# Kernel tuning notes

Measured on AMD Instinct MI355X. Metric: run time of the kernel, lower is better.

Reference implementation:

```python
import jax, jax.numpy as jnp
import numpy as np

B, S, D, H = 4, 2048, 512, 8
HD = D // H


def rotate_half(t):
    half = t.shape[-1] // 2
    return jnp.concatenate([-t[..., half:], t[..., :half]], axis=-1)


def setup_inputs() -> dict:
    key = jax.random.key(0)
    ks = jax.random.split(key, 8)
    x = jax.random.normal(ks[0], (B, S, D), dtype=jnp.float32)
    # realistic rotary tables built from angles
    inv_freq = 1.0 / (10000.0 ** (jnp.arange(0, D // 2, dtype=jnp.float32) / (D // 2)))
    ang = jnp.arange(S, dtype=jnp.float32)[:, None] * inv_freq[None, :]  # [S, D/2]
    ang = jnp.concatenate([ang, ang], axis=-1)  # [S, D]
    cos_emb = jnp.cos(ang)[None]  # [1, S, D]
    sin_emb = jnp.sin(ang)[None]
    mask = jax.random.randint(ks[1], (B, S, S), 0, 2).astype(jnp.bool_)
    scale = 1.0 / np.sqrt(D)
    wq = jax.random.normal(ks[2], (D, D), dtype=jnp.float32) * scale
    wk = jax.random.normal(ks[3], (D, D), dtype=jnp.float32) * scale
    wv = jax.random.normal(ks[4], (D, D), dtype=jnp.float32) * scale
    wo = jax.random.normal(ks[5], (D, D), dtype=jnp.float32) * scale
    return {"x": x, "cos_emb": cos_emb, "sin_emb": sin_emb, "mask": mask,
            "wq": wq, "wk": wk, "wv": wv, "wo": wo}


def reference(x, cos_emb, sin_emb, mask, wq, wk, wv, wo):
    bsz, seqlen, dim = x.shape
    # projections (weights stored as [in, out])
    xq = x @ wq
    xk = x @ wk
    xv = x @ wv
    # RoPE applied over full dim before head split (as in original)
    xq = xq * cos_emb + rotate_half(xq) * sin_emb
    xk = xk * cos_emb + rotate_half(xk) * sin_emb
    # split heads: [B, H, S, HD]
    xq = xq.reshape(bsz, seqlen, H, HD).transpose(0, 2, 1, 3)
    xk = xk.reshape(bsz, seqlen, H, HD).transpose(0, 2, 1, 3)
    xv = xv.reshape(bsz, seqlen, H, HD).transpose(0, 2, 1, 3)
    scores = jnp.einsum('bhqd,bhkd->bhqk', xq, xk) / jnp.sqrt(jnp.float32(HD))
    scores = scores + (~mask)[:, None].astype(scores.dtype) * (-1e9)
    scores = jax.nn.softmax(scores.astype(jnp.float32), axis=-1).astype(xq.dtype)
    scores = scores * mask[:, None].astype(scores.dtype)
    out = jnp.einsum('bhqk,bhkd->bhqd', scores, xv)
    out = out.transpose(0, 2, 1, 3).reshape(bsz, seqlen, dim)
    return out @ wo
```

## Files before the change

### kernel.cpp

```cpp
#include <hip/hip_runtime.h>
#include <hip/hip_bf16.h>

typedef __bf16 bf16x8 __attribute__((ext_vector_type(8)));
typedef float f32x4 __attribute__((ext_vector_type(4)));
typedef short short8 __attribute__((ext_vector_type(8)));

#define MFMA16(a, b, c) __builtin_amdgcn_mfma_f32_16x16x32_bf16((a), (b), (c), 0, 0, 0)

static constexpr int S = 2048;
static constexpr int D = 512;
static constexpr int HD = 64;
static constexpr int KBLK = 64;
#define QSCALE 0.18033688011112042f

typedef __attribute__((address_space(1))) const unsigned int gu32;
typedef __attribute__((address_space(3))) unsigned int lu32;

__device__ __forceinline__ void gll16(const void* g, void* l) {
  __builtin_amdgcn_global_load_lds((gu32*)g, (lu32*)l, 16, 0, 0);
}

__device__ __forceinline__ unsigned short f2b(float f) {
  return __builtin_bit_cast(unsigned short, __float2bfloat16(f));
}
__device__ __forceinline__ float b2f(unsigned short u) {
  return __builtin_bit_cast(float, (unsigned)u << 16);
}

__global__ void prep_kernel(const float* __restrict__ x, unsigned short* __restrict__ xb,
                            const int* __restrict__ m, unsigned long long* __restrict__ bits,
                            const float* __restrict__ wq, const float* __restrict__ wk,
                            const float* __restrict__ wv, const float* __restrict__ wo,
                            unsigned short* __restrict__ wqkvT, unsigned short* __restrict__ woT) {
  __shared__ float t[64][65];
  const int blk = blockIdx.x;
  const int tid = threadIdx.x;
  if (blk < 4096) {
    int idx = blk * 256 + tid;
    float4 v = ((const float4*)x)[idx];
    ushort4 o;
    o.x = f2b(v.x); o.y = f2b(v.y); o.z = f2b(v.z); o.w = f2b(v.w);
    ((ushort4*)xb)[idx] = o;
  } else if (blk < 6144) {
    const int stride = 2048 * 256;
    const int lane0 = (tid & 63) == 0;
    for (int gid = (blk - 4096) * 256 + tid; gid < 4 * 2048 * 2048; gid += stride) {
      unsigned long long w = __ballot(m[gid] != 0);
      if (lane0) bits[gid >> 6] = w;
    }
  } else {
    const int tt = blk - 6144;
    const int z = tt >> 6, r = tt & 63;
    const float* w = (z == 0) ? wq : (z == 1) ? wk : (z == 2) ? wv : wo;
    unsigned short* dst = (z < 3) ? wqkvT + (size_t)z * 512 * 512 : woT;
    const int i0 = (r & 7) * 64, o0 = (r >> 3) * 64;
    for (int it = 0; it < 16; ++it) {
      int idx = it * 256 + tid;
      int ii = idx >> 6, oo = idx & 63;
      t[oo][ii] = w[(size_t)(i0 + ii) * 512 + o0 + oo];
    }
    __syncthreads();
    for (int it = 0; it < 16; ++it) {
      int idx = it * 256 + tid;
      int oo = idx >> 6, ii = idx & 63;
      dst[(size_t)(o0 + oo) * 512 + i0 + ii] = f2b(t[oo][ii]);
    }
  }
}

__global__ __launch_bounds__(256)
void gemm2(const unsigned short* __restrict__ A, const unsigned short* __restrict__ Bt,
           int M, int N, int K, float* __restrict__ Cf,
           unsigned short* __restrict__ qd, unsigned short* __restrict__ kd,
           unsigned short* __restrict__ vtd, int mode) {
  __shared__ alignas(16) unsigned char smem[36864];
  unsigned short (*lds)[2][4096] = (unsigned short (*)[2][4096])smem;
  const int tid = threadIdx.x;
  const int lane = tid & 63, l15 = lane & 15, lg = lane >> 4;
  const int wave = tid >> 6;
  const int m0 = blockIdx.x * 128, n0 = blockIdx.y * 128;
  const int wm = (wave >> 1) * 64, wn = (wave & 1) * 64;
  const int wbase = wave * 512;
  const int grow = tid >> 2, gcol = (tid & 3) * 8;
  f32x4 acc[4][4] = {};
  const int nt = K / 32;

#define GSTAGE(sb, kk)                                                              \
  do {                                                                              \
    gll16(&A[(size_t)(m0 + grow) * K + (kk) + gcol], &lds[sb][0][wbase]);           \
    gll16(&A[(size_t)(m0 + 64 + grow) * K + (kk) + gcol], &lds[sb][0][2048 + wbase]);\
    gll16(&Bt[(size_t)(n0 + grow) * K + (kk) + gcol], &lds[sb][1][wbase]);          \
    gll16(&Bt[(size_t)(n0 + 64 + grow) * K + (kk) + gcol], &lds[sb][1][2048 + wbase]);\
  } while (0)

  GSTAGE(0, 0);
  asm volatile("s_waitcnt vmcnt(0)" ::: "memory");
  __syncthreads();
  for (int t = 0; t < nt; ++t) {
    const int cur = t & 1;
    if (t + 1 < nt) GSTAGE(cur ^ 1, (t + 1) * 32);
    bf16x8 af[4], bfr[4];
#pragma unroll
    for (int i = 0; i < 4; ++i) {
      af[i]  = *(const bf16x8*)&lds[cur][0][(wm + i * 16 + l15) * 32 + lg * 8];
      bfr[i] = *(const bf16x8*)&lds[cur][1][(wn + i * 16 + l15) * 32 + lg * 8];
    }
    __builtin_amdgcn_s_setprio(1);
#pragma unroll
    for (int i = 0; i < 4; ++i)
#pragma unroll
      for (int j = 0; j < 4; ++j)
        acc[i][j] = MFMA16(af[i], bfr[j], acc[i][j]);
    __builtin_amdgcn_s_setprio(0);
    asm volatile("s_waitcnt vmcnt(0)" ::: "memory");
    __syncthreads();
  }
#undef GSTAGE

  if (mode == 0) {
#pragma unroll
    for (int i = 0; i < 4; ++i)
#pragma unroll
      for (int j = 0; j < 4; ++j)
#pragma unroll
        for (int r = 0; r < 4; ++r)
          Cf[(size_t)(m0 + wm + i * 16 + lg * 4 + r) * N + (n0 + wn + j * 16 + l15)] = acc[i][j][r];
  } else {
    const int sel = n0 >> 9;
    const int nb = (n0 & 511) + wn;
    if (sel < 2) {
      unsigned short* dst = (sel == 0) ? qd : kd;
#pragma unroll
      for (int i = 0; i < 4; ++i)
#pragma unroll
        for (int j = 0; j < 4; ++j)
#pragma unroll
          for (int r = 0; r < 4; ++r) {
            const int m = m0 + wm + i * 16 + lg * 4 + r;
            const int nn = nb + j * 16 + l15;
            dst[(((size_t)(m >> 11) * 8 + (nn >> 6)) * 2048 + (m & 2047)) * 64 + (nn & 63)] =
                f2b(acc[i][j][r]);
          }
    } else {
      unsigned short* tb = (unsigned short*)smem + wave * 4608;
#pragma unroll
      for (int i = 0; i < 4; ++i)
#pragma unroll
        for (int j = 0; j < 4; ++j) {
          ushort4 pk;
          pk.x = f2b(acc[i][j][0]); pk.y = f2b(acc[i][j][1]);
          pk.z = f2b(acc[i][j][2]); pk.w = f2b(acc[i][j][3]);
          *(ushort4*)&tb[(j * 16 + l15) * 72 + i * 16 + lg * 4] = pk;
        }
      const int b0 = m0 >> 11;
      const int s0 = (m0 & 2047) + wm;
      const int g = lane >> 3, c = lane & 7;
#pragma unroll
      for (int rr = 0; rr < 8; ++rr) {
        const int row = rr * 8 + g;
        const int nng = nb + row;
        uint4 v = *(const uint4*)&tb[row * 72 + c * 8];
        *(uint4*)&vtd[(((size_t)(b0 * 8) + (nng >> 6)) * 64 + (nng & 63)) * 2048 + s0 + c * 8] = v;
      }
    }
  }
}

__global__ void rope_pair_kernel(const unsigned short* __restrict__ qpre, const unsigned short* __restrict__ kpre,
                                 const float* __restrict__ cose, const float* __restrict__ sine,
                                 unsigned short* __restrict__ qb, unsigned short* __restrict__ kb) {
  const int idx = blockIdx.x * 256 + threadIdx.x;
  const int hd0 = (idx & 7) * 8;
  const int rr = idx >> 3;
  const int b = rr >> 13, h = (rr >> 11) & 3, s = rr & 2047;
  const size_t lo = ((size_t)(b * 8 + h) * 2048 + s) * 64 + hd0;
  const size_t hi = lo + (size_t)4 * 2048 * 64;
  const int d0 = h * 64 + hd0;
  short8 qlo = *(const short8*)&qpre[lo];
  short8 qhi = *(const short8*)&qpre[hi];
  short8 klo = *(const short8*)&kpre[lo];
  short8 khi = *(const short8*)&kpre[hi];
  float4 c0 = *(const float4*)&cose[(size_t)s * 512 + d0];
  float4 c1 = *(const float4*)&cose[(size_t)s * 512 + d0 + 4];
  float4 s0 = *(const float4*)&sine[(size_t)s * 512 + d0];
  float4 s1 = *(const float4*)&sine[(size_t)s * 512 + d0 + 4];
  float cc[8] = {c0.x, c0.y, c0.z, c0.w, c1.x, c1.y, c1.z, c1.w};
  float ss[8] = {s0.x, s0.y, s0.z, s0.w, s1.x, s1.y, s1.z, s1.w};
  short8 qolo, qohi, kolo, kohi;
#pragma unroll
  for (int j = 0; j < 8; ++j) {
    float ql = b2f((unsigned short)qlo[j]), qh = b2f((unsigned short)qhi[j]);
    float kl = b2f((unsigned short)klo[j]), kh = b2f((unsigned short)khi[j]);
    qolo[j] = (short)f2b((ql * cc[j] - qh * ss[j]) * QSCALE);
    qohi[j] = (short)f2b((qh * cc[j] + ql * ss[j]) * QSCALE);
    kolo[j] = (short)f2b(kl * cc[j] - kh * ss[j]);
    kohi[j] = (short)f2b(kh * cc[j] + kl * ss[j]);
  }
  *(short8*)&qb[lo] = qolo;
  *(short8*)&qb[hi] = qohi;
  *(short8*)&kb[lo] = kolo;
  *(short8*)&kb[hi] = kohi;
}

__global__ __launch_bounds__(512)
void flash_kernel(const unsigned short* __restrict__ qb, const unsigned short* __restrict__ kb,
                  const unsigned short* __restrict__ vtb, const unsigned long long* __restrict__ mbits,
                  unsigned short* __restrict__ op0, unsigned short* __restrict__ op1,
                  float* __restrict__ ls0, float* __restrict__ ls1) {
  __shared__ alignas(16) unsigned short kv[2][2][4096];
  __shared__ alignas(16) f32x4 btab[16];
  const int tid = threadIdx.x;
  const int wave = tid >> 6, lane = tid & 63;
  const int l15 = lane & 15, lg = lane >> 4;
  const int swz = (l15 & 7) << 4;
  const int wgid = blockIdx.x;
  const int slot = wgid >> 3;
  const int bh = (wgid & 7) * 4 + (slot & 3);
  const int rest = slot >> 2;
  const int kh = rest & 1;
  const int q0 = (rest >> 1) * 256 + wave * 16;
  const int b = bh >> 3, h = bh & 7;
  const int kbase = kh * 1024;
  const unsigned short* Q = qb + ((size_t)bh * S + q0) * HD;
  const unsigned short* Kp = kb + (size_t)bh * S * HD;
  const unsigned short* Vt = vtb + (size_t)bh * HD * S;
  const unsigned long long* MrowA = mbits + ((size_t)b * S + q0 + l15) * (S / 64) + kh * 16;
  const unsigned long long* MrowB = MrowA + (size_t)128 * (S / 64);
  unsigned short* opart = kh ? op1 : op0;
  float* lsum = kh ? ls1 : ls0;

  const int srow = tid >> 3;
  const int scol = ((tid & 7) ^ (srow & 7)) * 8;
  const int ksrow = ((srow & 15) >> 2) * 8 + ((srow >> 4) & 1) * 4 + (srow & 3) + (srow >> 5) * 32;
  const int wbase = wave * 512;

  if (tid < 16) {
    f32x4 e;
    e[0] = (tid & 1) ? 0.f : -300.f;
    e[1] = (tid & 2) ? 0.f : -300.f;
    e[2] = (tid & 4) ? 0.f : -300.f;
    e[3] = (tid & 8) ? 0.f : -300.f;
    btab[tid] = e;
  }

  bf16x8 qf0a = *(const bf16x8*)&Q[l15 * HD + lg * 8];
  bf16x8 qf1a = *(const bf16x8*)&Q[l15 * HD + 32 + lg * 8];
  bf16x8 qf0b = *(const bf16x8*)&Q[(128 + l15) * HD + lg * 8];
  bf16x8 qf1b = *(const bf16x8*)&Q[(128 + l15) * HD + 32 + lg * 8];
  f32x4 oa[4] = {}, ob[4] = {};
  float lpa = 0.f, lpb = 0.f;
  const int lgs8 = lg * 8;

  unsigned long long wAa = MrowA[0], wAb = MrowB[0];
  gll16(&Kp[(size_t)(kbase + ksrow) * HD + scol], &kv[0][0][wbase]);
  gll16(&Vt[(size_t)srow * S + kbase + scol], &kv[0][1][wbase]);
  asm volatile("s_waitcnt vmcnt(0) lgkmcnt(0)" ::: "memory");
  __syncthreads();

  for (int t = 0; t < 16; ++t) {
    const int cur = t & 1;
    unsigned long long wBa = 0, wBb = 0;
    if (t + 1 < 16) {
      const int kn = kbase + (t + 1) * KBLK;
      gll16(&Kp[(size_t)(kn + ksrow) * HD + scol], &kv[cur ^ 1][0][wbase]);
      gll16(&Vt[(size_t)srow * S + kn + scol], &kv[cur ^ 1][1][wbase]);
      wBa = MrowA[t + 1];
      wBb = MrowB[t + 1];
    }
    const char* kbp = (const char*)&kv[cur][0][0];
    const char* vbp = (const char*)&kv[cur][1][0];

    bf16x8 pf0a, pf1a, pf0b, pf1b;
#pragma unroll
    for (int n = 0; n < 4; ++n) {
      const int cb = (n * 16 + l15) * 128 + ((lg * 16) ^ swz);
      bf16x8 kf0 = *(const bf16x8*)(kbp + cb);
      bf16x8 kf1 = *(const bf16x8*)(kbp + (cb ^ 64));
      f32x4 scA = {}, scB = {};
      __builtin_amdgcn_s_setprio(1);
      scA = MFMA16(kf0, qf0a, scA);
      scA = MFMA16(kf1, qf1a, scA);
      scB = MFMA16(kf0, qf0b, scB);
      scB = MFMA16(kf1, qf1b, scB);
      __builtin_amdgcn_s_setprio(0);
      const int sh = (n == 0) ? 0 : (n == 1) ? 4 : (n == 2) ? 32 : 36;
      const f32x4 ba = btab[(unsigned)(wAa >> (lgs8 + sh)) & 15u];
      const f32x4 bb = btab[(unsigned)(wAb >> (lgs8 + sh)) & 15u];
      f32x4 pa, pb;
#pragma unroll
      for (int r = 0; r < 4; ++r) {
        pa[r] = __builtin_amdgcn_exp2f(scA[r] + ba[r]);
        pb[r] = __builtin_amdgcn_exp2f(scB[r] + bb[r]);
      }
      lpa += (pa[0] + pa[1]) + (pa[2] + pa[3]);
      lpb += (pb[0] + pb[1]) + (pb[2] + pb[3]);
      bf16x8& dsta = (n < 2) ? pf0a : pf1a;
      bf16x8& dstb = (n < 2) ? pf0b : pf1b;
      const int jo = (n & 1) * 4;
#pragma unroll
      for (int j = 0; j < 4; ++j) {
        dsta[jo + j] = (__bf16)pa[j];
        dstb[jo + j] = (__bf16)pb[j];
      }
    }

    __builtin_amdgcn_s_setprio(1);
#pragma unroll
    for (int n = 0; n < 4; ++n) {
      const int cb = (n * 16 + l15) * 128 + ((lg * 16) ^ swz);
      bf16x8 vf0 = *(const bf16x8*)(vbp + cb);
      bf16x8 vf1 = *(const bf16x8*)(vbp + (cb ^ 64));
      oa[n] = MFMA16(pf0a, vf0, oa[n]);
      oa[n] = MFMA16(pf1a, vf1, oa[n]);
      ob[n] = MFMA16(pf0b, vf0, ob[n]);
      ob[n] = MFMA16(pf1b, vf1, ob[n]);
    }
    __builtin_amdgcn_s_setprio(0);

    asm volatile("s_waitcnt vmcnt(0)" ::: "memory");
    __syncthreads();
    wAa = wBa;
    wAb = wBb;
  }

  lpa += __shfl_xor(lpa, 16);
  lpa += __shfl_xor(lpa, 32);
  lpb += __shfl_xor(lpb, 16);
  lpb += __shfl_xor(lpb, 32);
  if (lg == 0) {
    lsum[(size_t)bh * S + q0 + l15] = lpa;
    lsum[(size_t)bh * S + q0 + 128 + l15] = lpb;
  }
#pragma unroll
  for (int r = 0; r < 4; ++r)
#pragma unroll
    for (int n = 0; n < 4; ++n) {
      opart[((size_t)(b * S + q0 + lg * 4 + r)) * D + h * HD + n * 16 + l15] = f2b(oa[n][r]);
      opart[((size_t)(b * S + q0 + 128 + lg * 4 + r)) * D + h * HD + n * 16 + l15] = f2b(ob[n][r]);
    }
}

__global__ __launch_bounds__(256)
void gemm_fused(const unsigned short* __restrict__ op0, const unsigned short* __restrict__ op1,
                const float* __restrict__ ls0, const float* __restrict__ ls1,
                const unsigned short* __restrict__ Bt, float* __restrict__ C) {
  __shared__ alignas(16) unsigned short ldsA[2][2048];
  __shared__ alignas(16) unsigned short ldsB[2][4096];
  __shared__ float invt[512];
  const int tid = threadIdx.x;
  const int lane = tid & 63, l15 = lane & 15, lg = lane >> 4;
  const int wave = tid >> 6;
  const int m0 = blockIdx.x * 64, n0 = blockIdx.y * 128;
  const int wm = (wave >> 1) * 32, wn = (wave & 1) * 64;
  const int wbase = wave * 512;
  const int grow = tid >> 2, gcol = (tid & 3) * 8;
  const size_t abase = (size_t)(m0 + (tid >> 2)) * 512 + (tid & 3) * 8;
  f32x4 acc[2][4] = {};

  for (int e = tid; e < 512; e += 256) {
    const int row = e >> 3, hh = e & 7;
    const int m = m0 + row;
    const size_t li = ((size_t)((m >> 11) * 8 + hh)) * 2048 + (m & 2047);
    const float l = ls0[li] + ls1[li];
    invt[e] = (l > 0.f) ? 1.f / l : 0.f;
  }

#define BSTAGE(sb, kk)                                                               \
  do {                                                                               \
    gll16(&Bt[(size_t)(n0 + grow) * 512 + (kk) + gcol], &ldsB[sb][wbase]);           \
    gll16(&Bt[(size_t)(n0 + 64 + grow) * 512 + (kk) + gcol], &ldsB[sb][2048 + wbase]);\
  } while (0)

  short8 a8, p8;
#define ALOAD(kk)                                          \
  do {                                                     \
    a8 = *(const short8*)&op0[abase + (kk)];               \
    p8 = *(const short8*)&op1[abase + (kk)];               \
  } while (0)

#define AWRITE(sb, kk)                                                                   \
  do {                                                                                   \
    const float inv = invt[((tid >> 2) << 3) | ((kk) >> 6)];                             \
    short8 pk;                                                                           \
    pk[0] = (short)f2b((b2f((unsigned short)a8[0]) + b2f((unsigned short)p8[0])) * inv); \
    pk[1] = (short)f2b((b2f((unsigned short)a8[1]) + b2f((unsigned short)p8[1])) * inv); \
    pk[2] = (short)f2b((b2f((unsigned short)a8[2]) + b2f((unsigned short)p8[2])) * inv); \
    pk[3] = (short)f2b((b2f((unsigned short)a8[3]) + b2f((unsigned short)p8[3])) * inv); \
    pk[4] = (short)f2b((b2f((unsigned short)a8[4]) + b2f((unsigned short)p8[4])) * inv); \
    pk[5] = (short)f2b((b2f((unsigned short)a8[5]) + b2f((unsigned short)p8[5])) * inv); \
    pk[6] = (short)f2b((b2f((unsigned short)a8[6]) + b2f((unsigned short)p8[6])) * inv); \
    pk[7] = (short)f2b((b2f((unsigned short)a8[7]) + b2f((unsigned short)p8[7])) * inv); \
    *(short8*)&ldsA[sb][(tid >> 2) * 32 + (tid & 3) * 8] = pk;                           \
  } while (0)

  ALOAD(0);
  BSTAGE(0, 0);
  __syncthreads();
  AWRITE(0, 0);
  __syncthreads();

  for (int t = 0; t < 16; ++t) {
    const int cur = t & 1;
    const bool have = (t + 1 < 16);
    if (have) { ALOAD((t + 1) * 32); BSTAGE(cur ^ 1, (t + 1) * 32); }
    bf16x8 af[2], bfr[4];
#pragma unroll
    for (int i = 0; i < 2; ++i)
      af[i] = *(const bf16x8*)&ldsA[cur][(wm + i * 16 + l15) * 32 + lg * 8];
#pragma unroll
    for (int j = 0; j < 4; ++j)
      bfr[j] = *(const bf16x8*)&ldsB[cur][(wn + j * 16 + l15) * 32 + lg * 8];
    __builtin_amdgcn_s_setprio(1);
#pragma unroll
    for (int i = 0; i < 2; ++i)
#pragma unroll
      for (int j = 0; j < 4; ++j)
        acc[i][j] = MFMA16(af[i], bfr[j], acc[i][j]);
    __builtin_amdgcn_s_setprio(0);
    asm volatile("s_waitcnt vmcnt(0)" ::: "memory");
    __syncthreads();
    if (have) AWRITE(cur ^ 1, (t + 1) * 32);
    __syncthreads();
  }
#undef BSTAGE
#undef ALOAD
#undef AWRITE

#pragma unroll
  for (int i = 0; i < 2; ++i)
#pragma unroll
    for (int j = 0; j < 4; ++j)
#pragma unroll
      for (int r = 0; r < 4; ++r)
        C[(size_t)(m0 + wm + i * 16 + lg * 4 + r) * 512 + (n0 + wn + j * 16 + l15)] = acc[i][j][r];
}

extern "C" void kernel_launch(void* const* d_in, const int* in_sizes, int n_in,
                              void* d_out, int out_size, void* d_ws, size_t ws_size,
                              hipStream_t stream) {
  const float* x = (const float*)d_in[0];
  const float* cose = (const float*)d_in[1];
  const float* sine = (const float*)d_in[2];
  const int* mask = (const int*)d_in[3];
  const float* wq = (const float*)d_in[4];
  const float* wk = (const float*)d_in[5];
  const float* wv = (const float*)d_in[6];
  const float* wo = (const float*)d_in[7];
  float* out = (float*)d_out;
  char* ws = (char*)d_ws;

  unsigned short* xb    = (unsigned short*)(ws);
  unsigned short* wqkvT = (unsigned short*)(ws + 8388608);
  unsigned short* woT   = (unsigned short*)(ws + 9961472);
  unsigned short* qpre  = (unsigned short*)(ws + 10485760);
  unsigned short* kpre  = (unsigned short*)(ws + 18874368);
  unsigned short* qbh   = (unsigned short*)(ws + 35651584);
  unsigned short* kbh   = (unsigned short*)(ws + 44040192);
  unsigned short* vtb   = (unsigned short*)(ws + 52428800);
  unsigned long long* mbits = (unsigned long long*)(ws + 60817408);
  unsigned short* op0 = (unsigned short*)(ws + 10485760);
  unsigned short* op1 = (unsigned short*)(ws + 62914560);
  float* ls0 = (float*)(ws + 79691776);
  float* ls1 = (float*)(ws + 79953920);

  prep_kernel<<<6400, 256, 0, stream>>>(x, xb, mask, mbits, wq, wk, wv, wo, wqkvT, woT);
  gemm2<<<dim3(64, 12), 256, 0, stream>>>(xb, wqkvT, 8192, 1536, 512, nullptr, qpre, kpre, vtb, 1);
  rope_pair_kernel<<<1024, 256, 0, stream>>>(qpre, kpre, cose, sine, qbh, kbh);
  flash_kernel<<<512, 512, 0, stream>>>(qbh, kbh, vtb, mbits, op0, op1, ls0, ls1);
  gemm_fused<<<dim3(128, 4), 256, 0, stream>>>(op0, op1, ls0, ls1, woT, out);
}
```

Baseline: 111.6 us.

## Fuse RoPE into QKV GEMM epilogue via permuted weight columns

Permutes the Q/K weight output columns during prep so that each GEMM wave tile holds both rotate-half partners of a dimension. RoPE and the Q scale are then applied in the GEMM epilogue, and the separate rope kernel is removed. This drops one launch and the bf16 round-trip of pre-RoPE Q/K through global memory. In exchange the epilogue does scalar, less coalesced cos/sin loads and 2-byte scattered stores.

```diff
diff --git a/kernel.cpp b/kernel.cpp
--- a/kernel.cpp
+++ b/kernel.cpp
@@ -63,27 +63,34 @@
     for (int it = 0; it < 16; ++it) {
       int idx = it * 256 + tid;
       int oo = idx >> 6, ii = idx & 63;
-      dst[(size_t)(o0 + oo) * 512 + i0 + ii] = f2b(t[oo][ii]);
+      int o = o0 + oo, od;
+      if (z < 2) {
+        const int hh = o >> 6, ff = (o >> 5) & 1, cc = o & 31;
+        od = ((hh & 3) * 2 + ff) * 64 + ((hh >> 2) << 5) + cc;
+      } else {
+        od = o;
+      }
+      dst[(size_t)od * 512 + i0 + ii] = f2b(t[oo][ii]);
     }
   }
 }
 
 __global__ __launch_bounds__(256)
 void gemm2(const unsigned short* __restrict__ A, const unsigned short* __restrict__ Bt,
-           int M, int N, int K, float* __restrict__ Cf,
+           const float* __restrict__ cose, const float* __restrict__ sine,
            unsigned short* __restrict__ qd, unsigned short* __restrict__ kd,
-           unsigned short* __restrict__ vtd, int mode) {
+           unsigned short* __restrict__ vtd) {
   __shared__ alignas(16) unsigned char smem[36864];
   unsigned short (*lds)[2][4096] = (unsigned short (*)[2][4096])smem;
   const int tid = threadIdx.x;
   const int lane = tid & 63, l15 = lane & 15, lg = lane >> 4;
   const int wave = tid >> 6;
+  const int K = 512;
   const int m0 = blockIdx.x * 128, n0 = blockIdx.y * 128;
   const int wm = (wave >> 1) * 64, wn = (wave & 1) * 64;
   const int wbase = wave * 512;
   const int grow = tid >> 2, gcol = (tid & 3) * 8;
   f32x4 acc[4][4] = {};
-  const int nt = K / 32;
 
 #define GSTAGE(sb, kk)                                                              \
   do {                                                                              \
@@ -96,9 +103,9 @@
   GSTAGE(0, 0);
   asm volatile("s_waitcnt vmcnt(0)" ::: "memory");
   __syncthreads();
-  for (int t = 0; t < nt; ++t) {
+  for (int t = 0; t < 16; ++t) {
     const int cur = t & 1;
-    if (t + 1 < nt) GSTAGE(cur ^ 1, (t + 1) * 32);
+    if (t + 1 < 16) GSTAGE(cur ^ 1, (t + 1) * 32);
     bf16x8 af[4], bfr[4];
 #pragma unroll
     for (int i = 0; i < 4; ++i) {
@@ -117,89 +124,52 @@
   }
 #undef GSTAGE
 
-  if (mode == 0) {
+  const int sel = n0 >> 9;
+  const int nb = (n0 & 511) + wn;
+  const int b0 = m0 >> 11;
+  if (sel < 2) {
+    unsigned short* dst = (sel == 0) ? qd : kd;
+    const float qs = (sel == 0) ? QSCALE : 1.f;
+    const int g = nb >> 6, p = g >> 1, f = g & 1;
+    const int sbase = (m0 & 2047) + wm;
 #pragma unroll
     for (int i = 0; i < 4; ++i)
 #pragma unroll
-      for (int j = 0; j < 4; ++j)
-#pragma unroll
-        for (int r = 0; r < 4; ++r)
-          Cf[(size_t)(m0 + wm + i * 16 + lg * 4 + r) * N + (n0 + wn + j * 16 + l15)] = acc[i][j][r];
+      for (int jl = 0; jl < 2; ++jl) {
+        const int c = jl * 16 + l15;
+        const int dtr = p * 64 + f * 32 + c;
+        const int hd = f * 32 + c;
+#pragma unroll
+        for (int r = 0; r < 4; ++r) {
+          const int s = sbase + i * 16 + lg * 4 + r;
+          const float cs = cose[(size_t)s * 512 + dtr];
+          const float sn = sine[(size_t)s * 512 + dtr];
+          const float lo = acc[i][jl][r], hi = acc[i][jl + 2][r];
+          dst[(((size_t)(b0 * 8) + p) * 2048 + s) * 64 + hd] = f2b((lo * cs - hi * sn) * qs);
+          dst[(((size_t)(b0 * 8) + p + 4) * 2048 + s) * 64 + hd] = f2b((hi * cs + lo * sn) * qs);
+        }
+      }
   } else {
-    const int sel = n0 >> 9;
-    const int nb = (n0 & 511) + wn;
-    if (sel < 2) {
-      unsigned short* dst = (sel == 0) ? qd : kd;
-#pragma unroll
-      for (int i = 0; i < 4; ++i)
-#pragma unroll
-        for (int j = 0; j < 4; ++j)
-#pragma unroll
-          for (int r = 0; r < 4; ++r) {
-            const int m = m0 + wm + i * 16 + lg * 4 + r;
-            const int nn = nb + j * 16 + l15;
-            dst[(((size_t)(m >> 11) * 8 + (nn >> 6)) * 2048 + (m & 2047)) * 64 + (nn & 63)] =
-                f2b(acc[i][j][r]);
-          }
-    } else {
-      unsigned short* tb = (unsigned short*)smem + wave * 4608;
-#pragma unroll
-      for (int i = 0; i < 4; ++i)
-#pragma unroll
-        for (int j = 0; j < 4; ++j) {
-          ushort4 pk;
-          pk.x = f2b(acc[i][j][0]); pk.y = f2b(acc[i][j][1]);
-          pk.z = f2b(acc[i][j][2]); pk.w = f2b(acc[i][j][3]);
-          *(ushort4*)&tb[(j * 16 + l15) * 72 + i * 16 + lg * 4] = pk;
-        }
-      const int b0 = m0 >> 11;
-      const int s0 = (m0 & 2047) + wm;
-      const int g = lane >> 3, c = lane & 7;
-#pragma unroll
-      for (int rr = 0; rr < 8; ++rr) {
-        const int row = rr * 8 + g;
-        const int nng = nb + row;
-        uint4 v = *(const uint4*)&tb[row * 72 + c * 8];
-        *(uint4*)&vtd[(((size_t)(b0 * 8) + (nng >> 6)) * 64 + (nng & 63)) * 2048 + s0 + c * 8] = v;
+    unsigned short* tb = (unsigned short*)smem + wave * 4608;
+#pragma unroll
+    for (int i = 0; i < 4; ++i)
+#pragma unroll
+      for (int j = 0; j < 4; ++j) {
+        ushort4 pk;
+        pk.x = f2b(acc[i][j][0]); pk.y = f2b(acc[i][j][1]);
+        pk.z = f2b(acc[i][j][2]); pk.w = f2b(acc[i][j][3]);
+        *(ushort4*)&tb[(j * 16 + l15) * 72 + i * 16 + lg * 4] = pk;
       }
-    }
-  }
-}
-
-__global__ void rope_pair_kernel(const unsigned short* __restrict__ qpre, const unsigned short* __restrict__ kpre,
-                                 const float* __restrict__ cose, const float* __restrict__ sine,
-                                 unsigned short* __restrict__ qb, unsigned short* __restrict__ kb) {
-  const int idx = blockIdx.x * 256 + threadIdx.x;
-  const int hd0 = (idx & 7) * 8;
-  const int rr = idx >> 3;
-  const int b = rr >> 13, h = (rr >> 11) & 3, s = rr & 2047;
-  const size_t lo = ((size_t)(b * 8 + h) * 2048 + s) * 64 + hd0;
-  const size_t hi = lo + (size_t)4 * 2048 * 64;
-  const int d0 = h * 64 + hd0;
-  short8 qlo = *(const short8*)&qpre[lo];
-  short8 qhi = *(const short8*)&qpre[hi];
-  short8 klo = *(const short8*)&kpre[lo];
-  short8 khi = *(const short8*)&kpre[hi];
-  float4 c0 = *(const float4*)&cose[(size_t)s * 512 + d0];
-  float4 c1 = *(const float4*)&cose[(size_t)s * 512 + d0 + 4];
-  float4 s0 = *(const float4*)&sine[(size_t)s * 512 + d0];
-  float4 s1 = *(const float4*)&sine[(size_t)s * 512 + d0 + 4];
-  float cc[8] = {c0.x, c0.y, c0.z, c0.w, c1.x, c1.y, c1.z, c1.w};
-  float ss[8] = {s0.x, s0.y, s0.z, s0.w, s1.x, s1.y, s1.z, s1.w};
-  short8 qolo, qohi, kolo, kohi;
-#pragma unroll
-  for (int j = 0; j < 8; ++j) {
-    float ql = b2f((unsigned short)qlo[j]), qh = b2f((unsigned short)qhi[j]);
-    float kl = b2f((unsigned short)klo[j]), kh = b2f((unsigned short)khi[j]);
-    qolo[j] = (short)f2b((ql * cc[j] - qh * ss[j]) * QSCALE);
-    qohi[j] = (short)f2b((qh * cc[j] + ql * ss[j]) * QSCALE);
-    kolo[j] = (short)f2b(kl * cc[j] - kh * ss[j]);
-    kohi[j] = (short)f2b(kh * cc[j] + kl * ss[j]);
-  }
-  *(short8*)&qb[lo] = qolo;
-  *(short8*)&qb[hi] = qohi;
-  *(short8*)&kb[lo] = kolo;
-  *(short8*)&kb[hi] = kohi;
+    const int s0 = (m0 & 2047) + wm;
+    const int g = lane >> 3, c = lane & 7;
+#pragma unroll
+    for (int rr = 0; rr < 8; ++rr) {
+      const int row = rr * 8 + g;
+      const int nng = nb + row;
+      uint4 v = *(const uint4*)&tb[row * 72 + c * 8];
+      *(uint4*)&vtd[(((size_t)(b0 * 8) + (nng >> 6)) * 64 + (nng & 63)) * 2048 + s0 + c * 8] = v;
+    }
+  }
 }
 
 __global__ __launch_bounds__(512)
@@ -452,8 +422,6 @@
   unsigned short* xb    = (unsigned short*)(ws);
   unsigned short* wqkvT = (unsigned short*)(ws + 8388608);
   unsigned short* woT   = (unsigned short*)(ws + 9961472);
-  unsigned short* qpre  = (unsigned short*)(ws + 10485760);
-  unsigned short* kpre  = (unsigned short*)(ws + 18874368);
   unsigned short* qbh   = (unsigned short*)(ws + 35651584);
   unsigned short* kbh   = (unsigned short*)(ws + 44040192);
   unsigned short* vtb   = (unsigned short*)(ws + 52428800);
@@ -464,8 +432,7 @@
   float* ls1 = (float*)(ws + 79953920);
 
   prep_kernel<<<6400, 256, 0, stream>>>(x, xb, mask, mbits, wq, wk, wv, wo, wqkvT, woT);
-  gemm2<<<dim3(64, 12), 256, 0, stream>>>(xb, wqkvT, 8192, 1536, 512, nullptr, qpre, kpre, vtb, 1);
-  rope_pair_kernel<<<1024, 256, 0, stream>>>(qpre, kpre, cose, sine, qbh, kbh);
+  gemm2<<<dim3(64, 12), 256, 0, stream>>>(xb, wqkvT, cose, sine, qbh, kbh, vtb);
   flash_kernel<<<512, 512, 0, stream>>>(qbh, kbh, vtb, mbits, op0, op1, ls0, ls1);
   gemm_fused<<<dim3(128, 4), 256, 0, stream>>>(op0, op1, ls0, ls1, woT, out);
 }
```

Result: faster. 107.8 us, median of 2 (-3.4%).
